# Optimization experiments

Measured on AMD Instinct MI355X. Metric: run time of the kernel, lower is better.

## Reference

```python
import jax, jax.numpy as jnp
import numpy as np

B, S, D, E, K = 4, 4096, 4096, 64, 2
TEMP = 1.0  # temperature=1.0 -> scale by 1/temperature kept for faithfulness


def setup_inputs() -> dict:
    key = jax.random.key(0)
    k1, k2 = jax.random.split(key)
    x = jax.random.normal(k1, (B, S, D), dtype=jnp.float32)
    W_gate = jax.random.normal(k2, (E, D), dtype=jnp.float32) * (D ** -0.5)
    return {"x": x, "W_gate": W_gate}


def reference(x, W_gate):
    # gate: Linear(d_model, n_experts, bias=False) -> logits [B,S,E]
    logits = jnp.einsum('bsd,ed->bse', x, W_gate)
    # temperature scaling (eval mode: no jitter / expert dropout / gumbel)
    logits = logits * (1.0 / TEMP)
    probs_full = jax.nn.softmax(logits, axis=-1)           # [B,S,E]
    topk_vals, idx = jax.lax.top_k(logits, K)              # [B,S,K]
    scores = jax.nn.softmax(topk_vals, axis=-1)            # renormalized top-k gates
    # z-loss: mean(logsumexp(logits)^2)
    z = jax.nn.logsumexp(logits, axis=-1)                  # [B,S]
    z_loss = jnp.mean(z * z)
    # aux stats (computed under no_grad in the original)
    importance = jax.lax.stop_gradient(jnp.mean(probs_full, axis=(0, 1)))  # [E]
    idx_flat = idx.reshape(-1)
    counts = jnp.zeros((E,), probs_full.dtype).at[idx_flat].add(1.0)       # [E]
    load = jax.lax.stop_gradient(counts / jnp.maximum(jnp.sum(counts), 1.0))
    return (idx, scores, probs_full, z_loss, importance, load)
```

## Files before the change

### kernel.cpp

```cpp
#include <hip/hip_runtime.h>

namespace {
constexpr int D = 4096;
constexpr int E = 64;
constexpr int M = 16384;
constexpr int BM = 64;
constexpr int BK = 64;
constexpr int NT = D / BK;
constexpr int NBLK = M / BM;

constexpr int OFF_IDX = 0;
constexpr int OFF_SCORES = 32768;
constexpr int OFF_PROBS = 65536;
constexpr int OFF_Z = 1114112;
constexpr int OFF_IMP = 1114113;
constexpr int OFF_LOAD = 1114177;

constexpr int WS_STRIDE = 132;
}

__device__ __forceinline__ void gload16(const float* g, float* l) {
  __builtin_amdgcn_global_load_lds(
      (const __attribute__((address_space(1))) void*)g,
      (__attribute__((address_space(3))) void*)l, 16, 0, 0);
}

__global__ __launch_bounds__(512, 2) void router_fused(
    const float* __restrict__ xg, const float* __restrict__ wg,
    float* __restrict__ out, float* __restrict__ ws) {
  __shared__ float smem[16384];

  const int t = threadIdx.x;
  const int u = t & 63;
  const int s = t >> 6;
  const int tx = u & 7;
  const int ty = u >> 3;
  const int r0 = blockIdx.x * BM;

  const int sw = s & 3;
  const float* gbase = (s < 4) ? (xg + (size_t)r0 * D) : wg;
  const int rA = sw * 16 + (u >> 4);
  const int tyA = sw * 2;
  const float* srcA = gbase + (size_t)rA * D + (((u & 15) ^ tyA) << 2);
  const float* srcB =
      gbase + (size_t)(rA + 8) * D + (((u & 15) ^ (tyA + 1)) << 2);
  const int dstoff = (s < 4 ? 0 : 4096) + sw * 1024;

  auto stage = [&](int r, float* buf) {
    const int rk = r * BK;
    float* dst = buf + dstoff;
    gload16(srcA + rk, dst);
    gload16(srcA + rk + (size_t)4 * D, dst + 256);
    gload16(srcB + rk, dst + 512);
    gload16(srcB + rk + (size_t)4 * D, dst + 768);
  };

  int xoff[2], woff[2];
#pragma unroll
  for (int kr = 0; kr < 2; ++kr) {
    const int kc = s * 2 + kr;
    xoff[kr] = ty * 512 + ((kc ^ ty) << 2);
    woff[kr] = 4096 + tx * 512 + ((kc ^ tx) << 2);
  }

  float acc[8][8];
#pragma unroll
  for (int i = 0; i < 8; ++i)
#pragma unroll
    for (int j = 0; j < 8; ++j) acc[i][j] = 0.f;

  stage(0, smem);

  for (int r = 0; r < NT; ++r) {
    __syncthreads();
    if (r + 1 < NT) stage(r + 1, smem + ((r + 1) & 1) * 8192);

    const float* buf = smem + (r & 1) * 8192;
#pragma unroll
    for (int kr = 0; kr < 2; ++kr) {
      float4 bw[8];
#pragma unroll
      for (int j = 0; j < 8; ++j)
        bw[j] = *(const float4*)&buf[woff[kr] + j * 64];
#pragma unroll
      for (int i = 0; i < 8; ++i) {
        const float4 ax = *(const float4*)&buf[xoff[kr] + i * 64];
#pragma unroll
        for (int j = 0; j < 8; ++j) {
          acc[i][j] = fmaf(ax.x, bw[j].x, acc[i][j]);
          acc[i][j] = fmaf(ax.y, bw[j].y, acc[i][j]);
          acc[i][j] = fmaf(ax.z, bw[j].z, acc[i][j]);
          acc[i][j] = fmaf(ax.w, bw[j].w, acc[i][j]);
        }
      }
    }
  }

  float v[8];
#pragma unroll
  for (int q = 0; q < 8; ++q) v[q] = 0.f;

#pragma unroll
  for (int ph = 0; ph < 2; ++ph) {
    __syncthreads();
    {
      float* P = smem;
      const int su2 = (s * 64 + u) * 2;
#pragma unroll
      for (int ii = 0; ii < 4; ++ii)
#pragma unroll
        for (int jj = 0; jj < 4; ++jj)
          *(float2*)&P[(ii * 4 + jj) * 1024 + su2] =
              make_float2(acc[ph * 4 + ii][2 * jj],
                          acc[ph * 4 + ii][2 * jj + 1]);
    }
    __syncthreads();
    if ((s >> 2) == ph) {
      const float* P = smem;
      const int base_p = (s & 3) * 4;
#pragma unroll
      for (int sl = 0; sl < 8; ++sl)
#pragma unroll
        for (int qq = 0; qq < 4; ++qq) {
          const float2 f =
              *(const float2*)&P[(base_p + qq) * 1024 + (sl * 64 + u) * 2];
          v[2 * qq] += f.x;
          v[2 * qq + 1] += f.y;
        }
    }
  }

  const int row = (u >> 3) * 8 + s;
  const int ebase = (u & 7) * 8;
  const int gr = r0 + row;

  __syncthreads();
  float* PW = smem;
  float* zw = smem + 512;
  int* cnt = (int*)(smem + 520);
  if (t < 64) cnt[t] = 0;
  __syncthreads();

  float v1 = v[0]; int i1 = ebase;
  float v2 = -3.402823466e+38f; int i2 = 0;
#pragma unroll
  for (int q = 1; q < 8; ++q) {
    const float x = v[q];
    if (x > v1) { v2 = v1; i2 = i1; v1 = x; i1 = ebase + q; }
    else if (x > v2) { v2 = x; i2 = ebase + q; }
  }
#pragma unroll
  for (int m = 1; m <= 4; m <<= 1) {
    const float o1 = __shfl_xor(v1, m);
    const int oi1 = __shfl_xor(i1, m);
    const float o2 = __shfl_xor(v2, m);
    const int oi2 = __shfl_xor(i2, m);
    if (o1 > v1 || (o1 == v1 && oi1 < i1)) {
      const bool c2 = (o2 > v1) || (o2 == v1 && oi2 < i1);
      v2 = c2 ? o2 : v1; i2 = c2 ? oi2 : i1;
      v1 = o1; i1 = oi1;
    } else if (o1 > v2 || (o1 == v2 && oi1 < i2)) {
      v2 = o1; i2 = oi1;
    }
  }

  float p[8];
  float ssum = 0.f;
#pragma unroll
  for (int q = 0; q < 8; ++q) { p[q] = __expf(v[q] - v1); ssum += p[q]; }
#pragma unroll
  for (int m = 1; m <= 4; m <<= 1) ssum += __shfl_xor(ssum, m);
  const float rs = 1.f / ssum;
#pragma unroll
  for (int q = 0; q < 8; ++q) p[q] *= rs;

  {
    const float4 o0 = {p[0], p[1], p[2], p[3]};
    const float4 o1 = {p[4], p[5], p[6], p[7]};
    *(float4*)&out[OFF_PROBS + (size_t)gr * 64 + ebase] = o0;
    *(float4*)&out[OFF_PROBS + (size_t)gr * 64 + ebase + 4] = o1;
  }
  const float z = v1 + __logf(ssum);
  const float z2 = z * z;

  if ((u & 7) == 0) {
    out[OFF_IDX + 2 * gr] = (float)i1;
    out[OFF_IDX + 2 * gr + 1] = (float)i2;
    const float e1 = __expf(v2 - v1);
    const float s0 = 1.f / (1.f + e1);
    out[OFF_SCORES + 2 * gr] = s0;
    out[OFF_SCORES + 2 * gr + 1] = e1 * s0;
    atomicAdd(&cnt[i1], 1);
    atomicAdd(&cnt[i2], 1);
  }

  float cs[8];
#pragma unroll
  for (int q = 0; q < 8; ++q) cs[q] = p[q];
#pragma unroll
  for (int m = 8; m <= 32; m <<= 1)
#pragma unroll
    for (int q = 0; q < 8; ++q) cs[q] += __shfl_xor(cs[q], m);
  float zs = z2;
#pragma unroll
  for (int m = 8; m <= 32; m <<= 1) zs += __shfl_xor(zs, m);
  if (u < 8) {
    const float4 c0 = {cs[0], cs[1], cs[2], cs[3]};
    const float4 c1 = {cs[4], cs[5], cs[6], cs[7]};
    *(float4*)&PW[s * 64 + u * 8] = c0;
    *(float4*)&PW[s * 64 + u * 8 + 4] = c1;
    if (u == 0) zw[s] = zs;
  }
  __syncthreads();

  if (t < 64) {
    float ic = 0.f;
#pragma unroll
    for (int w = 0; w < 8; ++w) ic += PW[w * 64 + t];
    ws[(size_t)blockIdx.x * WS_STRIDE + t] = ic;
    ws[(size_t)blockIdx.x * WS_STRIDE + 64 + t] = (float)cnt[t];
  } else if (t == 64) {
    float zz = 0.f;
#pragma unroll
    for (int w = 0; w < 8; ++w) zz += zw[w];
    ws[(size_t)blockIdx.x * WS_STRIDE + 128] = zz;
  }
}

__global__ __launch_bounds__(512) void router_reduce(
    const float* __restrict__ ws, float* __restrict__ out) {
  __shared__ float part[4][128];
  __shared__ float zp[4];
  const int t = threadIdx.x;
  const int c = t >> 7;
  const int slot = t & 127;
  float v = 0.f;
#pragma unroll 8
  for (int i = 0; i < 64; ++i)
    v += ws[(size_t)(c * 64 + i) * WS_STRIDE + slot];
  part[c][slot] = v;
  if (t < 4) {
    float zz = 0.f;
#pragma unroll 8
    for (int i = 0; i < 64; ++i)
      zz += ws[(size_t)(t * 64 + i) * WS_STRIDE + 128];
    zp[t] = zz;
  }
  __syncthreads();
  if (t < 128) {
    const float s4 = part[0][t] + part[1][t] + part[2][t] + part[3][t];
    if (t < 64)
      out[OFF_IMP + t] = s4 * (1.f / 16384.f);
    else
      out[OFF_LOAD + (t - 64)] = s4 * (1.f / 32768.f);
  } else if (t == 128) {
    out[OFF_Z] = (zp[0] + zp[1] + zp[2] + zp[3]) * (1.f / 16384.f);
  }
}

extern "C" void kernel_launch(void* const* d_in, const int* in_sizes, int n_in,
                              void* d_out, int out_size, void* d_ws, size_t ws_size,
                              hipStream_t stream) {
  const float* x = (const float*)d_in[0];
  const float* wgate = (const float*)d_in[1];
  float* out = (float*)d_out;
  float* ws = (float*)d_ws;

  router_fused<<<dim3(NBLK), dim3(512), 0, stream>>>(x, wgate, out, ws);
  router_reduce<<<dim3(1), dim3(512), 0, stream>>>(ws, out);
}
```

Before: 443.6 us.

## Halve row tile to 32 and raise occupancy to four blocks per CU

Cuts the rows per block from 64 to 32, doubling the grid to 512 blocks. Accumulators shrink to 4x8 per thread and LDS use per block drops, so launch bounds now allow four blocks per CU. The staging loads, split-K reduction, epilogue warp roles and final reduce are reworked to match. The aim is more blocks in flight to hide latency and to fill more CUs. The cost is more redundant loading of W_gate per block and lower arithmetic intensity per LDS read.

```diff
diff --git a/kernel.cpp b/kernel.cpp
--- a/kernel.cpp
+++ b/kernel.cpp
@@ -4,7 +4,7 @@
 constexpr int D = 4096;
 constexpr int E = 64;
 constexpr int M = 16384;
-constexpr int BM = 64;
+constexpr int BM = 32;
 constexpr int BK = 64;
 constexpr int NT = D / BK;
 constexpr int NBLK = M / BM;
@@ -25,10 +25,10 @@
       (__attribute__((address_space(3))) void*)l, 16, 0, 0);
 }
 
-__global__ __launch_bounds__(512, 2) void router_fused(
+__global__ __launch_bounds__(512, 4) void router_fused(
     const float* __restrict__ xg, const float* __restrict__ wg,
     float* __restrict__ out, float* __restrict__ ws) {
-  __shared__ float smem[16384];
+  __shared__ float smem[12288];
 
   const int t = threadIdx.x;
   const int u = t & 63;
@@ -37,35 +37,37 @@
   const int ty = u >> 3;
   const int r0 = blockIdx.x * BM;
 
-  const int sw = s & 3;
-  const float* gbase = (s < 4) ? (xg + (size_t)r0 * D) : wg;
-  const int rA = sw * 16 + (u >> 4);
-  const int tyA = sw * 2;
-  const float* srcA = gbase + (size_t)rA * D + (((u & 15) ^ tyA) << 2);
-  const float* srcB =
-      gbase + (size_t)(rA + 8) * D + (((u & 15) ^ (tyA + 1)) << 2);
-  const int dstoff = (s < 4 ? 0 : 4096) + sw * 1024;
-
+  const float* srcp[3];
+  int dstf[3];
+#pragma unroll
+  for (int j = 0; j < 3; ++j) {
+    const int c = 3 * s + j;
+    dstf[j] = c * 256;
+    if (c < 8) {
+      const int row = c * 4 + (u >> 4);
+      srcp[j] = xg + (size_t)(r0 + row) * D + (((u & 15) ^ c) << 2);
+    } else {
+      const int row = (c - 8) * 4 + (u >> 4);
+      srcp[j] = wg + (size_t)row * D + (((u & 15) ^ ((c - 8) >> 1)) << 2);
+    }
+  }
   auto stage = [&](int r, float* buf) {
     const int rk = r * BK;
-    float* dst = buf + dstoff;
-    gload16(srcA + rk, dst);
-    gload16(srcA + rk + (size_t)4 * D, dst + 256);
-    gload16(srcB + rk, dst + 512);
-    gload16(srcB + rk + (size_t)4 * D, dst + 768);
+#pragma unroll
+    for (int j = 0; j < 3; ++j) gload16(srcp[j] + rk, buf + dstf[j]);
   };
 
   int xoff[2], woff[2];
 #pragma unroll
   for (int kr = 0; kr < 2; ++kr) {
     const int kc = s * 2 + kr;
-    xoff[kr] = ty * 512 + ((kc ^ ty) << 2);
-    woff[kr] = 4096 + tx * 512 + ((kc ^ tx) << 2);
-  }
-
-  float acc[8][8];
-#pragma unroll
-  for (int i = 0; i < 8; ++i)
+    xoff[kr] = ty * 256 + ((kc ^ ty) << 2);
+    woff[kr] = 2048 + tx * 512 + ((kc ^ tx) << 2);
+  }
+
+  float acc[4][8];
+#pragma unroll
+  for (int i = 0; i < 4; ++i)
 #pragma unroll
     for (int j = 0; j < 8; ++j) acc[i][j] = 0.f;
 
@@ -73,9 +75,9 @@
 
   for (int r = 0; r < NT; ++r) {
     __syncthreads();
-    if (r + 1 < NT) stage(r + 1, smem + ((r + 1) & 1) * 8192);
-
-    const float* buf = smem + (r & 1) * 8192;
+    if (r + 1 < NT) stage(r + 1, smem + ((r + 1) & 1) * 6144);
+
+    const float* buf = smem + (r & 1) * 6144;
 #pragma unroll
     for (int kr = 0; kr < 2; ++kr) {
       float4 bw[8];
@@ -83,7 +85,7 @@
       for (int j = 0; j < 8; ++j)
         bw[j] = *(const float4*)&buf[woff[kr] + j * 64];
 #pragma unroll
-      for (int i = 0; i < 8; ++i) {
+      for (int i = 0; i < 4; ++i) {
         const float4 ax = *(const float4*)&buf[xoff[kr] + i * 64];
 #pragma unroll
         for (int j = 0; j < 8; ++j) {
@@ -107,17 +109,17 @@
       float* P = smem;
       const int su2 = (s * 64 + u) * 2;
 #pragma unroll
-      for (int ii = 0; ii < 4; ++ii)
+      for (int il = 0; il < 2; ++il)
 #pragma unroll
         for (int jj = 0; jj < 4; ++jj)
-          *(float2*)&P[(ii * 4 + jj) * 1024 + su2] =
-              make_float2(acc[ph * 4 + ii][2 * jj],
-                          acc[ph * 4 + ii][2 * jj + 1]);
+          *(float2*)&P[(il * 4 + jj) * 1024 + su2] =
+              make_float2(acc[ph * 2 + il][2 * jj],
+                          acc[ph * 2 + il][2 * jj + 1]);
     }
     __syncthreads();
-    if ((s >> 2) == ph) {
+    if (s < 4 && (s >> 1) == ph) {
       const float* P = smem;
-      const int base_p = (s & 3) * 4;
+      const int base_p = (s & 1) * 4;
 #pragma unroll
       for (int sl = 0; sl < 8; ++sl)
 #pragma unroll
@@ -130,100 +132,98 @@
     }
   }
 
-  const int row = (u >> 3) * 8 + s;
+  const int row = (u >> 3) * 4 + s;
   const int ebase = (u & 7) * 8;
   const int gr = r0 + row;
 
   __syncthreads();
   float* PW = smem;
-  float* zw = smem + 512;
-  int* cnt = (int*)(smem + 520);
+  float* zw = smem + 256;
+  int* cnt = (int*)(smem + 260);
   if (t < 64) cnt[t] = 0;
   __syncthreads();
 
-  float v1 = v[0]; int i1 = ebase;
-  float v2 = -3.402823466e+38f; int i2 = 0;
-#pragma unroll
-  for (int q = 1; q < 8; ++q) {
-    const float x = v[q];
-    if (x > v1) { v2 = v1; i2 = i1; v1 = x; i1 = ebase + q; }
-    else if (x > v2) { v2 = x; i2 = ebase + q; }
-  }
-#pragma unroll
-  for (int m = 1; m <= 4; m <<= 1) {
-    const float o1 = __shfl_xor(v1, m);
-    const int oi1 = __shfl_xor(i1, m);
-    const float o2 = __shfl_xor(v2, m);
-    const int oi2 = __shfl_xor(i2, m);
-    if (o1 > v1 || (o1 == v1 && oi1 < i1)) {
-      const bool c2 = (o2 > v1) || (o2 == v1 && oi2 < i1);
-      v2 = c2 ? o2 : v1; i2 = c2 ? oi2 : i1;
-      v1 = o1; i1 = oi1;
-    } else if (o1 > v2 || (o1 == v2 && oi1 < i2)) {
-      v2 = o1; i2 = oi1;
-    }
-  }
-
-  float p[8];
-  float ssum = 0.f;
-#pragma unroll
-  for (int q = 0; q < 8; ++q) { p[q] = __expf(v[q] - v1); ssum += p[q]; }
-#pragma unroll
-  for (int m = 1; m <= 4; m <<= 1) ssum += __shfl_xor(ssum, m);
-  const float rs = 1.f / ssum;
-#pragma unroll
-  for (int q = 0; q < 8; ++q) p[q] *= rs;
-
-  {
-    const float4 o0 = {p[0], p[1], p[2], p[3]};
-    const float4 o1 = {p[4], p[5], p[6], p[7]};
-    *(float4*)&out[OFF_PROBS + (size_t)gr * 64 + ebase] = o0;
-    *(float4*)&out[OFF_PROBS + (size_t)gr * 64 + ebase + 4] = o1;
-  }
-  const float z = v1 + __logf(ssum);
-  const float z2 = z * z;
-
-  if ((u & 7) == 0) {
-    out[OFF_IDX + 2 * gr] = (float)i1;
-    out[OFF_IDX + 2 * gr + 1] = (float)i2;
-    const float e1 = __expf(v2 - v1);
-    const float s0 = 1.f / (1.f + e1);
-    out[OFF_SCORES + 2 * gr] = s0;
-    out[OFF_SCORES + 2 * gr + 1] = e1 * s0;
-    atomicAdd(&cnt[i1], 1);
-    atomicAdd(&cnt[i2], 1);
-  }
-
-  float cs[8];
-#pragma unroll
-  for (int q = 0; q < 8; ++q) cs[q] = p[q];
-#pragma unroll
-  for (int m = 8; m <= 32; m <<= 1)
-#pragma unroll
-    for (int q = 0; q < 8; ++q) cs[q] += __shfl_xor(cs[q], m);
-  float zs = z2;
-#pragma unroll
-  for (int m = 8; m <= 32; m <<= 1) zs += __shfl_xor(zs, m);
-  if (u < 8) {
-    const float4 c0 = {cs[0], cs[1], cs[2], cs[3]};
-    const float4 c1 = {cs[4], cs[5], cs[6], cs[7]};
-    *(float4*)&PW[s * 64 + u * 8] = c0;
-    *(float4*)&PW[s * 64 + u * 8 + 4] = c1;
-    if (u == 0) zw[s] = zs;
+  if (s < 4) {
+    float v1 = v[0]; int i1 = ebase;
+    float v2 = -3.402823466e+38f; int i2 = 0;
+#pragma unroll
+    for (int q = 1; q < 8; ++q) {
+      const float x = v[q];
+      if (x > v1) { v2 = v1; i2 = i1; v1 = x; i1 = ebase + q; }
+      else if (x > v2) { v2 = x; i2 = ebase + q; }
+    }
+#pragma unroll
+    for (int m = 1; m <= 4; m <<= 1) {
+      const float o1 = __shfl_xor(v1, m);
+      const int oi1 = __shfl_xor(i1, m);
+      const float o2 = __shfl_xor(v2, m);
+      const int oi2 = __shfl_xor(i2, m);
+      if (o1 > v1 || (o1 == v1 && oi1 < i1)) {
+        const bool c2 = (o2 > v1) || (o2 == v1 && oi2 < i1);
+        v2 = c2 ? o2 : v1; i2 = c2 ? oi2 : i1;
+        v1 = o1; i1 = oi1;
+      } else if (o1 > v2 || (o1 == v2 && oi1 < i2)) {
+        v2 = o1; i2 = oi1;
+      }
+    }
+
+    float p[8];
+    float ssum = 0.f;
+#pragma unroll
+    for (int q = 0; q < 8; ++q) { p[q] = __expf(v[q] - v1); ssum += p[q]; }
+#pragma unroll
+    for (int m = 1; m <= 4; m <<= 1) ssum += __shfl_xor(ssum, m);
+    const float rs = 1.f / ssum;
+#pragma unroll
+    for (int q = 0; q < 8; ++q) p[q] *= rs;
+
+    {
+      const float4 o0 = {p[0], p[1], p[2], p[3]};
+      const float4 o1 = {p[4], p[5], p[6], p[7]};
+      *(float4*)&out[OFF_PROBS + (size_t)gr * 64 + ebase] = o0;
+      *(float4*)&out[OFF_PROBS + (size_t)gr * 64 + ebase + 4] = o1;
+    }
+    const float z = v1 + __logf(ssum);
+    const float z2 = z * z;
+
+    if ((u & 7) == 0) {
+      out[OFF_IDX + 2 * gr] = (float)i1;
+      out[OFF_IDX + 2 * gr + 1] = (float)i2;
+      const float e1 = __expf(v2 - v1);
+      const float s0 = 1.f / (1.f + e1);
+      out[OFF_SCORES + 2 * gr] = s0;
+      out[OFF_SCORES + 2 * gr + 1] = e1 * s0;
+      atomicAdd(&cnt[i1], 1);
+      atomicAdd(&cnt[i2], 1);
+    }
+
+    float cs[8];
+#pragma unroll
+    for (int q = 0; q < 8; ++q) cs[q] = p[q];
+#pragma unroll
+    for (int m = 8; m <= 32; m <<= 1)
+#pragma unroll
+      for (int q = 0; q < 8; ++q) cs[q] += __shfl_xor(cs[q], m);
+    float zs = z2;
+#pragma unroll
+    for (int m = 8; m <= 32; m <<= 1) zs += __shfl_xor(zs, m);
+    if (u < 8) {
+      const float4 c0 = {cs[0], cs[1], cs[2], cs[3]};
+      const float4 c1 = {cs[4], cs[5], cs[6], cs[7]};
+      *(float4*)&PW[s * 64 + u * 8] = c0;
+      *(float4*)&PW[s * 64 + u * 8 + 4] = c1;
+      if (u == 0) zw[s] = zs;
+    }
   }
   __syncthreads();
 
   if (t < 64) {
-    float ic = 0.f;
-#pragma unroll
-    for (int w = 0; w < 8; ++w) ic += PW[w * 64 + t];
+    const float ic =
+        PW[t] + PW[64 + t] + PW[128 + t] + PW[192 + t];
     ws[(size_t)blockIdx.x * WS_STRIDE + t] = ic;
     ws[(size_t)blockIdx.x * WS_STRIDE + 64 + t] = (float)cnt[t];
   } else if (t == 64) {
-    float zz = 0.f;
-#pragma unroll
-    for (int w = 0; w < 8; ++w) zz += zw[w];
-    ws[(size_t)blockIdx.x * WS_STRIDE + 128] = zz;
+    ws[(size_t)blockIdx.x * WS_STRIDE + 128] = zw[0] + zw[1] + zw[2] + zw[3];
   }
 }
 
@@ -236,14 +236,14 @@
   const int slot = t & 127;
   float v = 0.f;
 #pragma unroll 8
-  for (int i = 0; i < 64; ++i)
-    v += ws[(size_t)(c * 64 + i) * WS_STRIDE + slot];
+  for (int i = 0; i < 128; ++i)
+    v += ws[(size_t)(c * 128 + i) * WS_STRIDE + slot];
   part[c][slot] = v;
   if (t < 4) {
     float zz = 0.f;
 #pragma unroll 8
-    for (int i = 0; i < 64; ++i)
-      zz += ws[(size_t)(t * 64 + i) * WS_STRIDE + 128];
+    for (int i = 0; i < 128; ++i)
+      zz += ws[(size_t)(t * 128 + i) * WS_STRIDE + 128];
     zp[t] = zz;
   }
   __syncthreads();
```

Measured after the change: 412.8 us. 6.9% less time.
